# Performance work log

Measured on AMD Instinct MI355X. Metric: run time of the kernel, lower is better.

Reference implementation:

```python
import jax, jax.numpy as jnp
import numpy as np

B, S, E, DK = 4, 4096, 512, 64

def setup_inputs() -> dict:
    key = jax.random.key(0)
    ks = jax.random.split(key, 5)
    x = jax.random.normal(ks[0], (B, S, E), dtype=jnp.float32)
    context = jax.random.normal(ks[1], (B, S, E), dtype=jnp.float32)
    Wq = jax.random.normal(ks[2], (E, DK), dtype=jnp.float32) * 0.02
    Wk = jax.random.normal(ks[3], (E, DK), dtype=jnp.float32) * 0.02
    Wv = jax.random.normal(ks[4], (E, DK), dtype=jnp.float32) * 0.02
    return {"x": x, "context": context, "Wq": Wq, "Wk": Wk, "Wv": Wv}

def reference(x, context, Wq, Wk, Wv):
    # pad mask: 1 where the token embedding in x is not all-zero  [B,S,1]
    mask = 1.0 - jnp.all(x == 0, axis=2, keepdims=True).astype(x.dtype)
    Q = (x @ Wq) * mask          # [B,S,dk]
    K = (context @ Wk) * mask    # [B,S,dk]
    V = (context @ Wv) * mask    # [B,S,dk]
    energy = jnp.einsum('bqd,bkd->bqk', Q, K)  # [B,S,S]
    # original per-batch loop: length = #nonzero entries in first query row,
    # then columns >= length set to -inf (assumes trailing padding)
    lengths = jnp.sum(energy[:, 0, :] != 0, axis=-1)            # [B]
    col_valid = jnp.arange(S)[None, :] < lengths[:, None]       # [B,S]
    energy = jnp.where(col_valid[:, None, :], energy, -jnp.inf)
    score = jax.nn.softmax(energy / jnp.sqrt(jnp.asarray(DK, x.dtype)), axis=-1)
    return jnp.einsum('bqk,bkd->bqd', score, V) * mask
```

## Files before the change

### kernel.cpp

```cpp
#include <hip/hip_runtime.h>

constexpr int BB = 4;
constexpr int SS = 4096;
constexpr int EE = 512;
constexpr int BS = BB * SS;

typedef __attribute__((ext_vector_type(8))) short bf16x8;
typedef __attribute__((ext_vector_type(4))) float f32x4;
typedef unsigned long long ull;

union Frag {
  uint4 u4;
  unsigned int u[4];
  bf16x8 v;
};

__device__ __forceinline__ unsigned short f2bf(float f) {
  unsigned int u = __float_as_uint(f);
  unsigned int r = u + 0x7FFFu + ((u >> 16) & 1u);
  return (unsigned short)(r >> 16);
}
__device__ __forceinline__ float bf2f(unsigned short h) {
  return __uint_as_float(((unsigned int)h) << 16);
}
__device__ __forceinline__ unsigned int cvtpk(float a, float b) {
  unsigned int r;
  asm("v_cvt_pk_bf16_f32 %0, %1, %2" : "=v"(r) : "v"(a), "v"(b));
  return r;
}
__device__ __forceinline__ void gl16(const unsigned short* g, unsigned int* l) {
  __builtin_amdgcn_global_load_lds(
      (const __attribute__((address_space(1))) unsigned int*)(size_t)g,
      (__attribute__((address_space(3))) unsigned int*)(unsigned int)(size_t)l,
      16, 0, 0);
}
#define WAITVM(n) asm volatile("s_waitcnt vmcnt(" #n ")" ::: "memory")

__device__ __forceinline__ void split8(const float* v, uint4& H, uint4& L) {
  unsigned int hu[4], lu[4];
#pragma unroll
  for (int i = 0; i < 4; ++i) {
    unsigned int u0 = __float_as_uint(v[2 * i]);
    unsigned int u1 = __float_as_uint(v[2 * i + 1]);
    unsigned int h0 = u0 & 0xFFFF0000u, h1 = u1 & 0xFFFF0000u;
    hu[i] = (u0 >> 16) | h1;
    unsigned int r0 = __float_as_uint(v[2 * i] - __uint_as_float(h0));
    unsigned int r1 = __float_as_uint(v[2 * i + 1] - __uint_as_float(h1));
    lu[i] = (r0 >> 16) | (r1 & 0xFFFF0000u);
  }
  H = make_uint4(hu[0], hu[1], hu[2], hu[3]);
  L = make_uint4(lu[0], lu[1], lu[2], lu[3]);
}

__global__ __launch_bounds__(256) void mask_kernel(const float* __restrict__ x,
                                                   float* __restrict__ maskp) {
  const int row = blockIdx.x * 4 + (threadIdx.x >> 6);
  const int l = threadIdx.x & 63;
  const uint4* xr = (const uint4*)(x + (size_t)row * EE) + l;
  uint4 a = xr[0], b = xr[64];
  unsigned int o = (a.x | a.y | a.z | a.w | b.x | b.y | b.z | b.w) << 1;
  bool nz = __any(o != 0u);
  if (l == 0) maskp[row] = nz ? 1.0f : 0.0f;
}

__global__ __launch_bounds__(256, 2) void proj_kernel(
    const float* __restrict__ x, const float* __restrict__ ctx,
    const float* __restrict__ Wq, const float* __restrict__ Wk,
    const float* __restrict__ Wv, const float* __restrict__ maskp,
    unsigned short* __restrict__ Qb, unsigned short* __restrict__ Kb,
    unsigned short* __restrict__ Vt)
{
  __shared__ __align__(16) unsigned short Ah[2][64][40], Al[2][64][40];
  __shared__ __align__(16) unsigned short Wh[2][128][40], Wl[2][128][40];

  const int t = threadIdx.x;
  const int kvmode = blockIdx.y;
  const int r0g = blockIdx.x * 64;
  const int nlim = kvmode ? 8 : 4;

  const float* A = kvmode ? ctx : x;

  const int arow = t >> 2, akq = t & 3;
  const int wn = t & 127, wkq = t >> 7;
  const int wn6 = wn & 63;
  const float* Wg = kvmode ? ((wn < 64) ? Wk : Wv) : Wq;
  const float wscale = kvmode ? 1.0f : 0.18033688011112042f;
  const bool wact = kvmode || (wn < 64);

  float a8[8], w16[16];
  auto sload = [&](int kc) {
    const float* ap = A + (size_t)(r0g + arow) * EE + kc + akq * 8;
    *(float4*)&a8[0] = *(const float4*)ap;
    *(float4*)&a8[4] = *(const float4*)(ap + 4);
    if (wact) {
#pragma unroll
      for (int j = 0; j < 16; ++j)
        w16[j] = Wg[(size_t)(kc + wkq * 16 + j) * 64 + wn6] * wscale;
    }
  };
  auto swrite = [&](int buf) {
    uint4 H, L;
    split8(a8, H, L);
    *(uint4*)&Ah[buf][arow][akq * 8] = H;
    *(uint4*)&Al[buf][arow][akq * 8] = L;
    if (wact) {
      split8(w16, H, L);
      *(uint4*)&Wh[buf][wn][wkq * 16] = H;
      *(uint4*)&Wl[buf][wn][wkq * 16] = L;
      split8(w16 + 8, H, L);
      *(uint4*)&Wh[buf][wn][wkq * 16 + 8] = H;
      *(uint4*)&Wl[buf][wn][wkq * 16 + 8] = L;
    }
  };

  const int l = t & 63, wi = t >> 6, g = l >> 4, li = l & 15;
  f32x4 acc[8] = {};

  sload(0);
  swrite(0);
  int cur = 0;
  for (int c = 0; c < 16; ++c) {
    if (c < 15) sload((c + 1) * 32);
    __syncthreads();
    Frag ah, alo;
    ah.u4  = *(const uint4*)&Ah[cur][wi * 16 + li][g * 8];
    alo.u4 = *(const uint4*)&Al[cur][wi * 16 + li][g * 8];
#pragma unroll
    for (int nf = 0; nf < 8; ++nf) {
      if (nf < nlim) {
        Frag bh, bl;
        bh.u4 = *(const uint4*)&Wh[cur][nf * 16 + li][g * 8];
        bl.u4 = *(const uint4*)&Wl[cur][nf * 16 + li][g * 8];
        acc[nf] = __builtin_amdgcn_mfma_f32_16x16x32_bf16(ah.v, bh.v, acc[nf], 0, 0, 0);
        acc[nf] = __builtin_amdgcn_mfma_f32_16x16x32_bf16(alo.v, bh.v, acc[nf], 0, 0, 0);
        acc[nf] = __builtin_amdgcn_mfma_f32_16x16x32_bf16(ah.v, bl.v, acc[nf], 0, 0, 0);
      }
    }
    if (c < 15) swrite(cur ^ 1);
    cur ^= 1;
  }

  float mk[4];
  const int browbase = r0g + wi * 16 + g * 4;
#pragma unroll
  for (int r = 0; r < 4; ++r) mk[r] = maskp[browbase + r];
  if (kvmode) {
#pragma unroll
    for (int nf = 0; nf < 4; ++nf)
#pragma unroll
      for (int r = 0; r < 4; ++r)
        Kb[(size_t)(browbase + r) * 64 + nf * 16 + li] = f2bf(acc[nf][r] * mk[r]);
    const int bidx = r0g >> 12;
    const int sbase = (r0g & 4095) + wi * 16 + g * 4;
#pragma unroll
    for (int nf = 4; nf < 8; ++nf) {
      unsigned int u0 = cvtpk(acc[nf][0] * mk[0], acc[nf][1] * mk[1]);
      unsigned int u1 = cvtpk(acc[nf][2] * mk[2], acc[nf][3] * mk[3]);
      ull v = (ull)u0 | ((ull)u1 << 32);
      *(ull*)(Vt + ((size_t)(bidx * 64 + (nf - 4) * 16 + li)) * SS + sbase) = v;
    }
  } else {
#pragma unroll
    for (int nf = 0; nf < 4; ++nf)
#pragma unroll
      for (int r = 0; r < 4; ++r)
        Qb[(size_t)(browbase + r) * 64 + nf * 16 + li] = f2bf(acc[nf][r] * mk[r]);
  }
}

__global__ __launch_bounds__(256) void len_kernel(
    const unsigned short* __restrict__ Qb,
    const unsigned short* __restrict__ Kb,
    unsigned int* __restrict__ lenp)
{
  __shared__ float q0row[64];
  const int t = threadIdx.x;
  const int b = blockIdx.y;
  if (t < 64) q0row[t] = bf2f(Qb[(size_t)b * SS * 64 + t]);
  __syncthreads();
  const int k = blockIdx.x * 256 + t;
  const uint4* kr = (const uint4*)(Kb + ((size_t)(b * SS + k)) * 64);
  float acc = 0.f;
#pragma unroll
  for (int j = 0; j < 8; ++j) {
    uint4 u = kr[j];
    unsigned int w[4] = {u.x, u.y, u.z, u.w};
#pragma unroll
    for (int q = 0; q < 4; ++q) {
      acc = fmaf(q0row[j * 8 + q * 2],     __uint_as_float(w[q] << 16), acc);
      acc = fmaf(q0row[j * 8 + q * 2 + 1], __uint_as_float(w[q] & 0xFFFF0000u), acc);
    }
  }
  unsigned long long bal = __ballot(acc != 0.0f);
  if ((t & 63) == 0) atomicAdd(&lenp[b], (unsigned int)__popcll(bal));
}

template <bool MASKED>
__device__ __forceinline__ void tile_body(
    const unsigned int* ksb, const unsigned int* vsb, unsigned int* prow,
    const Frag& qf0, const Frag& qf1, f32x4* O, float& m_r, float& l_r,
    int l, int g, int li, int lim)
{
  f32x4 acc[4] = {};
#pragma unroll
  for (int f = 0; f < 2; ++f) {
    const bf16x8 qv = f ? qf1.v : qf0.v;
    const int oc = f * 4 + g;
#pragma unroll
    for (int a = 0; a < 4; ++a) {
      const int krow = a * 16 + li;
      Frag kf;
      kf.u4 = *(const uint4*)&ksb[krow * 32 + ((oc ^ (krow & 7)) << 2)];
      acc[a] = __builtin_amdgcn_mfma_f32_16x16x32_bf16(kf.v, qv, acc[a], 0, 0, 0);
    }
  }

  float pvv[4][4];
  float tm = -1e30f;
#pragma unroll
  for (int a = 0; a < 4; ++a)
#pragma unroll
    for (int r = 0; r < 4; ++r) {
      float v = acc[a][r];
      if (MASKED) v = (a * 16 + (g << 2) + r < lim) ? v : -1e30f;
      pvv[a][r] = v;
      tm = fmaxf(tm, v);
    }
  if (__any(tm > m_r + 8.f)) {
    float tq = fmaxf(tm, __shfl_xor(tm, 16));
    tq = fmaxf(tq, __shfl_xor(tq, 32));
    const float nm = fmaxf(m_r, tq);
    const float al = exp2f(m_r - nm);
    m_r = nm;
    l_r *= al;
    float alq[4];
#pragma unroll
    for (int r = 0; r < 4; ++r) alq[r] = __shfl(al, (l & 48) | (g << 2) | r);
#pragma unroll
    for (int o4 = 0; o4 < 4; ++o4)
#pragma unroll
      for (int r = 0; r < 4; ++r) O[o4][r] *= alq[r];
  }
  float rs = 0.f;
#pragma unroll
  for (int a = 0; a < 4; ++a)
#pragma unroll
    for (int r = 0; r < 4; ++r) {
      float e = exp2f(pvv[a][r] - m_r);
      pvv[a][r] = e;
      rs += e;
    }
  rs += __shfl_xor(rs, 16);
  rs += __shfl_xor(rs, 32);
  l_r += rs;

#pragma unroll
  for (int a = 0; a < 4; ++a) {
    prow[a * 8 + g * 2]     = cvtpk(pvv[a][0], pvv[a][1]);
    prow[a * 8 + g * 2 + 1] = cvtpk(pvv[a][2], pvv[a][3]);
  }
#pragma unroll
  for (int f = 0; f < 2; ++f) {
    Frag pf;
    pf.u4 = *(const uint4*)&prow[f * 16 + g * 4];
    const int oc = f * 4 + g;
#pragma unroll
    for (int o4 = 0; o4 < 4; ++o4) {
      const int vrow = o4 * 16 + li;
      Frag vf;
      vf.u4 = *(const uint4*)&vsb[vrow * 32 + ((oc ^ (vrow & 7)) << 2)];
      O[o4] = __builtin_amdgcn_mfma_f32_16x16x32_bf16(pf.v, vf.v, O[o4], 0, 0, 0);
    }
  }
}

template <int NW>
__global__ __launch_bounds__(NW * 64, (NW == 8) ? 4 : 3) void attn_kernel(
    const unsigned short* __restrict__ Qb,
    const unsigned short* __restrict__ Kb,
    const unsigned short* __restrict__ Vt,
    const unsigned int* __restrict__ lenp,
    float* __restrict__ Op, float* __restrict__ mlp, int kvChunk)
{
  __shared__ __align__(16) unsigned int ks[2][2048];
  __shared__ __align__(16) unsigned int vs[2][2048];
  __shared__ __align__(16) unsigned int ps[NW * 16 * 36];

  constexpr int SPW = 16 / NW;

  const int t  = threadIdx.x;
  const int l  = t & 63;
  const int wi = t >> 6;
  const int g  = l >> 4;
  const int li = l & 15;
  const int b  = blockIdx.z;
  const int sp = blockIdx.y;
  const int q0 = blockIdx.x * (NW * 16);

  const unsigned int len = lenp[b];
  const int kvS = sp * kvChunk;
  const int kvE = min((int)len, kvS + kvChunk);
  int rem = kvE - kvS; if (rem < 0) rem = 0;
  const int NF = rem >> 6;
  const int NT = NF + ((rem & 63) ? 1 : 0);

  Frag qf0, qf1;
  {
    const uint4* qg = (const uint4*)(Qb + ((size_t)(b * SS + q0 + wi * 16 + li)) * 64);
    qf0.u4 = qg[g];
    qf1.u4 = qg[4 + g];
  }

  f32x4 O[4] = {};
  float m_r = 0.f, l_r = 0.f;

  const int srow8 = l >> 3;
  const int sch = l & 7;
  auto issue = [&](int key0, int bufsel) {
#pragma unroll
    for (int s2 = 0; s2 < SPW; ++s2) {
      const int seg = wi * SPW + s2;
      const int s8 = seg & 7;
      const int row = s8 * 8 + srow8;
      if (seg < 8) {
        gl16(Kb + ((size_t)(b * SS + key0 + row)) * 64 + ((sch ^ (row & 7)) << 3),
             &ks[bufsel][s8 * 256]);
      } else {
        gl16(Vt + ((size_t)(b * 64 + row)) * SS + key0 + ((sch ^ (row & 7)) << 3),
             &vs[bufsel][s8 * 256]);
      }
    }
  };

  unsigned int* prow = &ps[(wi * 16 + li) * 36];
  int cur = 0;
  if (NT > 0) issue(kvS, 0);
  for (int tix = 0; tix < NT; ++tix) {
    const int key0 = kvS + (tix << 6);
    const bool last = (tix + 1 == NT);
    if (!last) {
      issue(key0 + 64, cur ^ 1);
      if constexpr (NW == 8) { WAITVM(2); } else { WAITVM(4); }
    } else {
      WAITVM(0);
    }
    __builtin_amdgcn_s_barrier();
    __builtin_amdgcn_sched_barrier(0);
    const int lim = kvE - key0;
    if (tix < NF)
      tile_body<false>(&ks[cur][0], &vs[cur][0], prow, qf0, qf1, O, m_r, l_r, l, g, li, lim);
    else
      tile_body<true>(&ks[cur][0], &vs[cur][0], prow, qf0, qf1, O, m_r, l_r, l, g, li, lim);
    __builtin_amdgcn_s_barrier();
    cur ^= 1;
  }

  const int qrow = q0 + wi * 16;
  if (g == 0) {
    mlp[(size_t)sp * 2 * BS + b * SS + qrow + li] = m_r;
    mlp[(size_t)sp * 2 * BS + BS + b * SS + qrow + li] = l_r;
  }
  const size_t obase = (size_t)sp * BS * 64;
#pragma unroll
  for (int o4 = 0; o4 < 4; ++o4)
#pragma unroll
    for (int r = 0; r < 4; ++r)
      Op[obase + ((size_t)(b * SS + qrow + (g << 2) + r)) * 64 + o4 * 16 + li] = O[o4][r];
}

template <int NS>
__global__ __launch_bounds__(256) void combine_kernel(
    const float* __restrict__ Op, const float* __restrict__ mlp,
    const float* __restrict__ maskp, float* __restrict__ out)
{
  const int i4 = blockIdx.x * 256 + threadIdx.x;
  const int e0 = i4 * 4;
  const int row = e0 >> 6;
  float ms[NS], lsv[NS];
#pragma unroll
  for (int s = 0; s < NS; ++s) {
    ms[s] = mlp[(size_t)s * 2 * BS + row];
    lsv[s] = mlp[(size_t)s * 2 * BS + BS + row];
  }
  float M = -1e30f;
#pragma unroll
  for (int s = 0; s < NS; ++s)
    if (lsv[s] > 0.f) M = fmaxf(M, ms[s]);
  float4 num = {0.f, 0.f, 0.f, 0.f};
  float den = 0.f;
#pragma unroll
  for (int s = 0; s < NS; ++s) {
    if (lsv[s] > 0.f) {
      const float w = exp2f(ms[s] - M);
      const float4 o = *(const float4*)(Op + (size_t)s * BS * 64 + e0);
      num.x += w * o.x; num.y += w * o.y; num.z += w * o.z; num.w += w * o.w;
      den += w * lsv[s];
    }
  }
  const float sc = (den > 0.f) ? maskp[row] / den : 0.f;
  float4 r = {num.x * sc, num.y * sc, num.z * sc, num.w * sc};
  *(float4*)(out + e0) = r;
}

extern "C" void kernel_launch(void* const* d_in, const int* in_sizes, int n_in,
                              void* d_out, int out_size, void* d_ws, size_t ws_size,
                              hipStream_t stream) {
  const float* x   = (const float*)d_in[0];
  const float* ctx = (const float*)d_in[1];
  const float* Wq  = (const float*)d_in[2];
  const float* Wk  = (const float*)d_in[3];
  const float* Wv  = (const float*)d_in[4];
  float* out = (float*)d_out;

  char* ws = (char*)d_ws;
  unsigned short* Qb = (unsigned short*)(ws);
  unsigned short* Kb = (unsigned short*)(ws + 2097152);
  unsigned short* Vt = (unsigned short*)(ws + 4194304);
  float* maskp       = (float*)(ws + 6291456);
  unsigned int* lenp = (unsigned int*)(ws + 6356992);
  const size_t base = 6357248ull;

  const size_t need4 = base + 4ull * 4194304 + 4ull * 131072;
  const size_t need2 = base + 2ull * 4194304 + 2ull * 131072;
  int nsplit = (ws_size >= need4) ? 4 : (ws_size >= need2) ? 2 : 1;

  float* Op  = (float*)(ws + base);
  float* mlp = (float*)(ws + base + (size_t)nsplit * 4194304);

  hipMemsetAsync(lenp, 0, 16, stream);
  mask_kernel<<<dim3(BS / 4), 256, 0, stream>>>(x, maskp);
  proj_kernel<<<dim3(BS / 64, 2), 256, 0, stream>>>(x, ctx, Wq, Wk, Wv, maskp, Qb, Kb, Vt);
  len_kernel<<<dim3(16, 4), 256, 0, stream>>>(Qb, Kb, lenp);
  if (nsplit == 4) {
    attn_kernel<8><<<dim3(SS / 128, 4, BB), 512, 0, stream>>>(Qb, Kb, Vt, lenp, Op, mlp, 1024);
    combine_kernel<4><<<dim3(BS * 64 / 1024), 256, 0, stream>>>(Op, mlp, maskp, out);
  } else if (nsplit == 2) {
    attn_kernel<4><<<dim3(SS / 64, 2, BB), 256, 0, stream>>>(Qb, Kb, Vt, lenp, Op, mlp, 2048);
    combine_kernel<2><<<dim3(BS * 64 / 1024), 256, 0, stream>>>(Op, mlp, maskp, out);
  } else {
    attn_kernel<4><<<dim3(SS / 64, 1, BB), 256, 0, stream>>>(Qb, Kb, Vt, lenp, Op, mlp, 4096);
    combine_kernel<1><<<dim3(BS * 64 / 1024), 256, 0, stream>>>(Op, mlp, maskp, out);
  }
}
```

Baseline: 170.0 us.

## Pre-split weights, drop LDS from projection, read V directly, raise KV split

Adds a prep kernel that splits weights into bf16 hi/lo pairs once. The projection then reads these directly from global memory with no shared-memory staging, as a templated kernel per Q or KV. The Q output skips the mask multiply, since the mask is now applied only in combine. The attention kernel stops staging V tiles in LDS and loads V fragments straight from global memory. It uses a fixed 512-thread block with higher occupancy and allows an 8-way KV split sized to the workspace. This trades LDS traffic and barriers for uncoalesced global loads of V and weights, which may raise memory latency.

Result: slower. 314.0 us (+84.7%).

```diff
diff --git a/kernel.cpp b/kernel.cpp
--- a/kernel.cpp
+++ b/kernel.cpp
@@ -63,88 +63,81 @@
   if (l == 0) maskp[row] = nz ? 1.0f : 0.0f;
 }
 
-__global__ __launch_bounds__(256, 2) void proj_kernel(
+__global__ __launch_bounds__(256) void prep_w(
+    const float* __restrict__ Wq, const float* __restrict__ Wk,
+    const float* __restrict__ Wv, unsigned short* __restrict__ Whl) {
+  const int m = blockIdx.x;
+  const int ng = blockIdx.y;
+  const int t = threadIdx.x;
+  const int n = ng * 4 + (t >> 6);
+  const int kl = t & 63;
+  const float* W = (m == 0) ? Wq : (m == 1) ? Wk : Wv;
+  const float sc = (m == 0) ? 0.18033688011112042f : 1.0f;
+#pragma unroll
+  for (int kc = 0; kc < 8; ++kc) {
+    const int k = kc * 64 + kl;
+    const float w = W[(size_t)k * 64 + n] * sc;
+    const unsigned int hu = __float_as_uint(w) & 0xFFFF0000u;
+    const float lo = w - __uint_as_float(hu);
+    Whl[((size_t)(m * 2 + 0) * 64 + n) * 512 + k] = (unsigned short)(hu >> 16);
+    Whl[((size_t)(m * 2 + 1) * 64 + n) * 512 + k] =
+        (unsigned short)(__float_as_uint(lo) >> 16);
+  }
+}
+
+template <int KV>
+__global__ __launch_bounds__(128) void proj_kernel(
     const float* __restrict__ x, const float* __restrict__ ctx,
-    const float* __restrict__ Wq, const float* __restrict__ Wk,
-    const float* __restrict__ Wv, const float* __restrict__ maskp,
+    const unsigned short* __restrict__ Whl, const float* __restrict__ maskp,
     unsigned short* __restrict__ Qb, unsigned short* __restrict__ Kb,
     unsigned short* __restrict__ Vt)
 {
-  __shared__ __align__(16) unsigned short Ah[2][64][40], Al[2][64][40];
-  __shared__ __align__(16) unsigned short Wh[2][128][40], Wl[2][128][40];
-
   const int t = threadIdx.x;
-  const int kvmode = blockIdx.y;
-  const int r0g = blockIdx.x * 64;
-  const int nlim = kvmode ? 8 : 4;
-
-  const float* A = kvmode ? ctx : x;
-
-  const int arow = t >> 2, akq = t & 3;
-  const int wn = t & 127, wkq = t >> 7;
-  const int wn6 = wn & 63;
-  const float* Wg = kvmode ? ((wn < 64) ? Wk : Wv) : Wq;
-  const float wscale = kvmode ? 1.0f : 0.18033688011112042f;
-  const bool wact = kvmode || (wn < 64);
-
-  float a8[8], w16[16];
-  auto sload = [&](int kc) {
-    const float* ap = A + (size_t)(r0g + arow) * EE + kc + akq * 8;
-    *(float4*)&a8[0] = *(const float4*)ap;
-    *(float4*)&a8[4] = *(const float4*)(ap + 4);
-    if (wact) {
-#pragma unroll
-      for (int j = 0; j < 16; ++j)
-        w16[j] = Wg[(size_t)(kc + wkq * 16 + j) * 64 + wn6] * wscale;
-    }
-  };
-  auto swrite = [&](int buf) {
+  const int l = t & 63, wi = t >> 6, g = l >> 4, li = l & 15;
+  const int r0g = blockIdx.x * 32;
+  const int row = r0g + wi * 16 + li;
+
+  const float* A = KV ? ctx : x;
+  const float* ap = A + (size_t)row * EE + g * 8;
+
+  f32x4 acc[KV ? 8 : 4] = {};
+  float a8[8];
+  *(float4*)&a8[0] = *(const float4*)(ap);
+  *(float4*)&a8[4] = *(const float4*)(ap + 4);
+
+  for (int c = 0; c < 16; ++c) {
     uint4 H, L;
     split8(a8, H, L);
-    *(uint4*)&Ah[buf][arow][akq * 8] = H;
-    *(uint4*)&Al[buf][arow][akq * 8] = L;
-    if (wact) {
-      split8(w16, H, L);
-      *(uint4*)&Wh[buf][wn][wkq * 16] = H;
-      *(uint4*)&Wl[buf][wn][wkq * 16] = L;
-      split8(w16 + 8, H, L);
-      *(uint4*)&Wh[buf][wn][wkq * 16 + 8] = H;
-      *(uint4*)&Wl[buf][wn][wkq * 16 + 8] = L;
-    }
-  };
-
-  const int l = t & 63, wi = t >> 6, g = l >> 4, li = l & 15;
-  f32x4 acc[8] = {};
-
-  sload(0);
-  swrite(0);
-  int cur = 0;
-  for (int c = 0; c < 16; ++c) {
-    if (c < 15) sload((c + 1) * 32);
-    __syncthreads();
+    if (c < 15) {
+      const float* ap2 = ap + (c + 1) * 32;
+      *(float4*)&a8[0] = *(const float4*)(ap2);
+      *(float4*)&a8[4] = *(const float4*)(ap2 + 4);
+    }
     Frag ah, alo;
-    ah.u4  = *(const uint4*)&Ah[cur][wi * 16 + li][g * 8];
-    alo.u4 = *(const uint4*)&Al[cur][wi * 16 + li][g * 8];
-#pragma unroll
-    for (int nf = 0; nf < 8; ++nf) {
-      if (nf < nlim) {
+    ah.u4 = H;
+    alo.u4 = L;
+    const int ko = c * 32 + g * 8;
+#pragma unroll
+    for (int mm = 0; mm < (KV ? 2 : 1); ++mm) {
+      const unsigned short* wb = Whl + ((size_t)((KV ? (1 + mm) : 0) * 2) * 64) * 512;
+#pragma unroll
+      for (int nf = 0; nf < 4; ++nf) {
         Frag bh, bl;
-        bh.u4 = *(const uint4*)&Wh[cur][nf * 16 + li][g * 8];
-        bl.u4 = *(const uint4*)&Wl[cur][nf * 16 + li][g * 8];
-        acc[nf] = __builtin_amdgcn_mfma_f32_16x16x32_bf16(ah.v, bh.v, acc[nf], 0, 0, 0);
-        acc[nf] = __builtin_amdgcn_mfma_f32_16x16x32_bf16(alo.v, bh.v, acc[nf], 0, 0, 0);
-        acc[nf] = __builtin_amdgcn_mfma_f32_16x16x32_bf16(ah.v, bl.v, acc[nf], 0, 0, 0);
+        bh.u4 = *(const uint4*)(wb + ((size_t)(nf * 16 + li)) * 512 + ko);
+        bl.u4 = *(const uint4*)(wb + ((size_t)(64 + nf * 16 + li)) * 512 + ko);
+        const int ai = mm * 4 + nf;
+        acc[ai] = __builtin_amdgcn_mfma_f32_16x16x32_bf16(ah.v, bh.v, acc[ai], 0, 0, 0);
+        acc[ai] = __builtin_amdgcn_mfma_f32_16x16x32_bf16(alo.v, bh.v, acc[ai], 0, 0, 0);
+        acc[ai] = __builtin_amdgcn_mfma_f32_16x16x32_bf16(ah.v, bl.v, acc[ai], 0, 0, 0);
       }
     }
-    if (c < 15) swrite(cur ^ 1);
-    cur ^= 1;
-  }
-
-  float mk[4];
+  }
+
   const int browbase = r0g + wi * 16 + g * 4;
-#pragma unroll
-  for (int r = 0; r < 4; ++r) mk[r] = maskp[browbase + r];
-  if (kvmode) {
+  if (KV) {
+    float mk[4];
+#pragma unroll
+    for (int r = 0; r < 4; ++r) mk[r] = maskp[browbase + r];
 #pragma unroll
     for (int nf = 0; nf < 4; ++nf)
 #pragma unroll
@@ -153,18 +146,18 @@
     const int bidx = r0g >> 12;
     const int sbase = (r0g & 4095) + wi * 16 + g * 4;
 #pragma unroll
-    for (int nf = 4; nf < 8; ++nf) {
-      unsigned int u0 = cvtpk(acc[nf][0] * mk[0], acc[nf][1] * mk[1]);
-      unsigned int u1 = cvtpk(acc[nf][2] * mk[2], acc[nf][3] * mk[3]);
-      ull v = (ull)u0 | ((ull)u1 << 32);
-      *(ull*)(Vt + ((size_t)(bidx * 64 + (nf - 4) * 16 + li)) * SS + sbase) = v;
+    for (int nf = 0; nf < 4; ++nf) {
+      const unsigned int u0 = cvtpk(acc[4 + nf][0] * mk[0], acc[4 + nf][1] * mk[1]);
+      const unsigned int u1 = cvtpk(acc[4 + nf][2] * mk[2], acc[4 + nf][3] * mk[3]);
+      const ull v = (ull)u0 | ((ull)u1 << 32);
+      *(ull*)(Vt + ((size_t)(bidx * 64 + nf * 16 + li)) * SS + sbase) = v;
     }
   } else {
 #pragma unroll
     for (int nf = 0; nf < 4; ++nf)
 #pragma unroll
       for (int r = 0; r < 4; ++r)
-        Qb[(size_t)(browbase + r) * 64 + nf * 16 + li] = f2bf(acc[nf][r] * mk[r]);
+        Qb[(size_t)(browbase + r) * 64 + nf * 16 + li] = f2bf(acc[nf][r]);
   }
 }
 
@@ -197,7 +190,7 @@
 
 template <bool MASKED>
 __device__ __forceinline__ void tile_body(
-    const unsigned int* ksb, const unsigned int* vsb, unsigned int* prow,
+    const unsigned int* ksb, const unsigned short* vtb, unsigned int* prow,
     const Frag& qf0, const Frag& qf1, f32x4* O, float& m_r, float& l_r,
     int l, int g, int li, int lim)
 {
@@ -215,7 +208,6 @@
     }
   }
 
-  float pvv[4][4];
   float tm = -1e30f;
 #pragma unroll
   for (int a = 0; a < 4; ++a)
@@ -223,7 +215,7 @@
     for (int r = 0; r < 4; ++r) {
       float v = acc[a][r];
       if (MASKED) v = (a * 16 + (g << 2) + r < lim) ? v : -1e30f;
-      pvv[a][r] = v;
+      acc[a][r] = v;
       tm = fmaxf(tm, v);
     }
   if (__any(tm > m_r + 8.f)) {
@@ -246,8 +238,8 @@
   for (int a = 0; a < 4; ++a)
 #pragma unroll
     for (int r = 0; r < 4; ++r) {
-      float e = exp2f(pvv[a][r] - m_r);
-      pvv[a][r] = e;
+      const float e = exp2f(acc[a][r] - m_r);
+      acc[a][r] = e;
       rs += e;
     }
   rs += __shfl_xor(rs, 16);
@@ -256,8 +248,8 @@
 
 #pragma unroll
   for (int a = 0; a < 4; ++a) {
-    prow[a * 8 + g * 2]     = cvtpk(pvv[a][0], pvv[a][1]);
-    prow[a * 8 + g * 2 + 1] = cvtpk(pvv[a][2], pvv[a][3]);
+    prow[a * 8 + g * 2]     = cvtpk(acc[a][0], acc[a][1]);
+    prow[a * 8 + g * 2 + 1] = cvtpk(acc[a][2], acc[a][3]);
   }
 #pragma unroll
   for (int f = 0; f < 2; ++f) {
@@ -266,16 +258,14 @@
     const int oc = f * 4 + g;
 #pragma unroll
     for (int o4 = 0; o4 < 4; ++o4) {
-      const int vrow = o4 * 16 + li;
       Frag vf;
-      vf.u4 = *(const uint4*)&vsb[vrow * 32 + ((oc ^ (vrow & 7)) << 2)];
+      vf.u4 = *(const uint4*)(vtb + (size_t)(o4 * 16 + li) * SS + oc * 8);
       O[o4] = __builtin_amdgcn_mfma_f32_16x16x32_bf16(pf.v, vf.v, O[o4], 0, 0, 0);
     }
   }
 }
 
-template <int NW>
-__global__ __launch_bounds__(NW * 64, (NW == 8) ? 4 : 3) void attn_kernel(
+__global__ __launch_bounds__(512, 8) void attn_kernel(
     const unsigned short* __restrict__ Qb,
     const unsigned short* __restrict__ Kb,
     const unsigned short* __restrict__ Vt,
@@ -283,10 +273,7 @@
     float* __restrict__ Op, float* __restrict__ mlp, int kvChunk)
 {
   __shared__ __align__(16) unsigned int ks[2][2048];
-  __shared__ __align__(16) unsigned int vs[2][2048];
-  __shared__ __align__(16) unsigned int ps[NW * 16 * 36];
-
-  constexpr int SPW = 16 / NW;
+  __shared__ __align__(16) unsigned int ps[8 * 16 * 36];
 
   const int t  = threadIdx.x;
   const int l  = t & 63;
@@ -295,7 +282,7 @@
   const int li = l & 15;
   const int b  = blockIdx.z;
   const int sp = blockIdx.y;
-  const int q0 = blockIdx.x * (NW * 16);
+  const int q0 = blockIdx.x * 128;
 
   const unsigned int len = lenp[b];
   const int kvS = sp * kvChunk;
@@ -314,33 +301,22 @@
   f32x4 O[4] = {};
   float m_r = 0.f, l_r = 0.f;
 
-  const int srow8 = l >> 3;
+  const int srow = wi * 8 + (l >> 3);
   const int sch = l & 7;
   auto issue = [&](int key0, int bufsel) {
-#pragma unroll
-    for (int s2 = 0; s2 < SPW; ++s2) {
-      const int seg = wi * SPW + s2;
-      const int s8 = seg & 7;
-      const int row = s8 * 8 + srow8;
-      if (seg < 8) {
-        gl16(Kb + ((size_t)(b * SS + key0 + row)) * 64 + ((sch ^ (row & 7)) << 3),
-             &ks[bufsel][s8 * 256]);
-      } else {
-        gl16(Vt + ((size_t)(b * 64 + row)) * SS + key0 + ((sch ^ (row & 7)) << 3),
-             &vs[bufsel][s8 * 256]);
-      }
-    }
+    gl16(Kb + ((size_t)(b * SS + key0 + srow)) * 64 + ((sch ^ (srow & 7)) << 3),
+         &ks[bufsel][wi * 256]);
   };
 
+  const unsigned short* vtbase = Vt + (size_t)b * 64 * SS;
   unsigned int* prow = &ps[(wi * 16 + li) * 36];
   int cur = 0;
   if (NT > 0) issue(kvS, 0);
   for (int tix = 0; tix < NT; ++tix) {
     const int key0 = kvS + (tix << 6);
-    const bool last = (tix + 1 == NT);
-    if (!last) {
+    if (tix + 1 < NT) {
       issue(key0 + 64, cur ^ 1);
-      if constexpr (NW == 8) { WAITVM(2); } else { WAITVM(4); }
+      WAITVM(1);
     } else {
       WAITVM(0);
     }
@@ -348,9 +324,9 @@
     __builtin_amdgcn_sched_barrier(0);
     const int lim = kvE - key0;
     if (tix < NF)
-      tile_body<false>(&ks[cur][0], &vs[cur][0], prow, qf0, qf1, O, m_r, l_r, l, g, li, lim);
+      tile_body<false>(&ks[cur][0], vtbase + key0, prow, qf0, qf1, O, m_r, l_r, l, g, li, lim);
     else
-      tile_body<true>(&ks[cur][0], &vs[cur][0], prow, qf0, qf1, O, m_r, l_r, l, g, li, lim);
+      tile_body<true>(&ks[cur][0], vtbase + key0, prow, qf0, qf1, O, m_r, l_r, l, g, li, lim);
     __builtin_amdgcn_s_barrier();
     cur ^= 1;
   }
@@ -418,27 +394,27 @@
   unsigned short* Vt = (unsigned short*)(ws + 4194304);
   float* maskp       = (float*)(ws + 6291456);
   unsigned int* lenp = (unsigned int*)(ws + 6356992);
-  const size_t base = 6357248ull;
-
-  const size_t need4 = base + 4ull * 4194304 + 4ull * 131072;
-  const size_t need2 = base + 2ull * 4194304 + 2ull * 131072;
-  int nsplit = (ws_size >= need4) ? 4 : (ws_size >= need2) ? 2 : 1;
+  unsigned short* Whl = (unsigned short*)(ws + 6357248);
+  const size_t base = 6357248ull + 393216ull;
+
+  const size_t sOp = 4194304ull, sMl = 131072ull;
+  int nsplit = (ws_size >= base + 8 * (sOp + sMl)) ? 8
+             : (ws_size >= base + 4 * (sOp + sMl)) ? 4
+             : (ws_size >= base + 2 * (sOp + sMl)) ? 2 : 1;
 
   float* Op  = (float*)(ws + base);
-  float* mlp = (float*)(ws + base + (size_t)nsplit * 4194304);
+  float* mlp = (float*)(ws + base + (size_t)nsplit * sOp);
 
   hipMemsetAsync(lenp, 0, 16, stream);
+  prep_w<<<dim3(3, 16), 256, 0, stream>>>(Wq, Wk, Wv, Whl);
+  proj_kernel<0><<<dim3(BS / 32), 128, 0, stream>>>(x, ctx, Whl, maskp, Qb, Kb, Vt);
   mask_kernel<<<dim3(BS / 4), 256, 0, stream>>>(x, maskp);
-  proj_kernel<<<dim3(BS / 64, 2), 256, 0, stream>>>(x, ctx, Wq, Wk, Wv, maskp, Qb, Kb, Vt);
+  proj_kernel<1><<<dim3(BS / 32), 128, 0, stream>>>(x, ctx, Whl, maskp, Qb, Kb, Vt);
   len_kernel<<<dim3(16, 4), 256, 0, stream>>>(Qb, Kb, lenp);
-  if (nsplit == 4) {
-    attn_kernel<8><<<dim3(SS / 128, 4, BB), 512, 0, stream>>>(Qb, Kb, Vt, lenp, Op, mlp, 1024);
-    combine_kernel<4><<<dim3(BS * 64 / 1024), 256, 0, stream>>>(Op, mlp, maskp, out);
-  } else if (nsplit == 2) {
-    attn_kernel<4><<<dim3(SS / 64, 2, BB), 256, 0, stream>>>(Qb, Kb, Vt, lenp, Op, mlp, 2048);
-    combine_kernel<2><<<dim3(BS * 64 / 1024), 256, 0, stream>>>(Op, mlp, maskp, out);
-  } else {
-    attn_kernel<4><<<dim3(SS / 64, 1, BB), 256, 0, stream>>>(Qb, Kb, Vt, lenp, Op, mlp, 4096);
-    combine_kernel<1><<<dim3(BS * 64 / 1024), 256, 0, stream>>>(Op, mlp, maskp, out);
-  }
-}
+  const int kvChunk = SS / nsplit;
+  attn_kernel<<<dim3(SS / 128, nsplit, BB), 512, 0, stream>>>(Qb, Kb, Vt, lenp, Op, mlp, kvChunk);
+  if (nsplit == 8)      combine_kernel<8><<<dim3(BS * 64 / 1024), 256, 0, stream>>>(Op, mlp, maskp, out);
+  else if (nsplit == 4) combine_kernel<4><<<dim3(BS * 64 / 1024), 256, 0, stream>>>(Op, mlp, maskp, out);
+  else if (nsplit == 2) combine_kernel<2><<<dim3(BS * 64 / 1024), 256, 0, stream>>>(Op, mlp, maskp, out);
+  else                  combine_kernel<1><<<dim3(BS * 64 / 1024), 256, 0, stream>>>(Op, mlp, maskp, out);
+}
```
